# Performance work log

Measured on AMD Instinct MI355X. Metric: run time of the kernel, lower is better.

The kernel has to match this reference:

```python
import jax, jax.numpy as jnp
import numpy as np

N = 64
K_CHEB = 5
EPS = 1e-5

# db4 decomposition filters (scaling_filter.mat Lo_D / Hi_D, length 8)
_LO = np.array([-0.010597401784997278, 0.032883011666982945, 0.030841381835986965,
                -0.18703481171888114, -0.02798376941698385, 0.6308807679295904,
                0.7148465705525415, 0.23037781330885523], dtype=np.float32)
_HI = np.array([-0.23037781330885523, 0.7148465705525415, -0.6308807679295904,
                -0.02798376941698385, 0.18703481171888114, 0.030841381835986965,
                0.032883011666982945, -0.010597401784997278], dtype=np.float32)
# torch stores np.flip(filters) and Conv2d does cross-correlation -> use flipped taps here too
_KERN = np.stack([_LO[::-1], _HI[::-1]])[:, None, None, :].copy()  # [2,1,1,8]


def _wavelet_step(x):
    # x: [B, C, 1, W]; circular pad 3 each side, depthwise len-8 conv, stride 2
    p = 3  # filter_length // 2 - 1
    xp = jnp.concatenate([x[..., -p:], x, x[..., :p]], axis=-1)
    b, c, h, wp = xp.shape
    out = jax.lax.conv_general_dilated(
        xp.reshape(b * c, 1, h, wp), jnp.asarray(_KERN), (1, 2), 'VALID',
        dimension_numbers=('NCHW', 'OIHW', 'NCHW'))
    out = out.reshape(b, c, 2, h, -1)
    return out[:, :, 0], out[:, :, 1]  # (approx, detail)


def _cbam(x, fc1, fc2, sa_w):
    # x: [B, 657, 1, 64]; channel attention then spatial attention
    def mlp(v):  # v: [B, C, 1, 1]
        h = jax.nn.relu(jnp.einsum('oc,bchw->bohw', fc1, v))
        return jnp.einsum('oc,bchw->bohw', fc2, h)
    avg = x.mean(axis=(2, 3), keepdims=True)
    mx = x.max(axis=(2, 3), keepdims=True)
    x = x * jax.nn.sigmoid(mlp(avg) + mlp(mx))
    s = jnp.concatenate([x.mean(axis=1, keepdims=True), x.max(axis=1, keepdims=True)], axis=1)
    sa = jax.nn.sigmoid(jax.lax.conv_general_dilated(
        s, sa_w, (1, 1), ((3, 3), (3, 3)), dimension_numbers=('NCHW', 'OIHW', 'NCHW')))
    return x * sa


def _global_edge_weight(w_tril, mask):
    xs, ys = np.tril_indices(N)
    E = jnp.zeros((N, N), w_tril.dtype).at[xs, ys].set(w_tril)
    E = E + E.T - jnp.diag(jnp.diag(E))
    return (E * mask).reshape(-1)


def _norm_adj(edges, w):
    # PyG NewSGConv.norm: add remaining self-loops (fill=1), deg from |w|, sym normalize
    row, col = edges[0], edges[1]
    has_self = jnp.zeros((N,), w.dtype).at[row].add(jnp.where(row == col, 1.0, 0.0)) > 0
    w_self = jnp.where(has_self, 0.0, 1.0).astype(w.dtype)
    deg = jnp.zeros((N,), w.dtype).at[row].add(jnp.abs(w)) + w_self
    dsafe = jnp.where(deg > 0, deg, 1.0)
    dinv = jnp.where(deg > 0, jax.lax.rsqrt(dsafe), 0.0)
    norm = dinv[row] * w * dinv[col]
    A = jnp.zeros((N, N), w.dtype).at[col, row].add(norm)  # out[i] = sum_j A[i,j] x[j]
    return A + jnp.diag(dinv * w_self * dinv)


def _gcn_block(x, A, W, b, g, be):
    # x: [B, N, C_in]; K-hop SGConv propagation, linear, train-mode batchnorm over (B, N)
    for _ in range(K_CHEB):
        x = jnp.einsum('ij,bjc->bic', A, x)
    x = x @ W.T + b
    mean = x.mean(axis=(0, 1))
    var = x.var(axis=(0, 1))
    return (x - mean) * jax.lax.rsqrt(var + EPS) * g + be


def _classify(x, W1, b1, g, be, W2, b2):
    out = x.reshape(x.shape[0], -1) @ W1.T + b1
    out = (out - out.mean(0)) * jax.lax.rsqrt(out.var(0) + EPS) * g + be
    return jax.nn.log_softmax(out @ W2.T + b2, axis=1)


def _forward(x, local_graph_weight, global_mask, ca_fc1, ca_fc2, sa_conv, edge_weight_tril,
             ld_W, ld_b, ld_g, ld_be, ld1_W, ld1_b, ld1_g, ld1_be,
             d_W, d_b, d_g, d_be, d1_W, d1_b, d1_g, d1_be,
             cls_W1, cls_b1, cls_g, cls_be, cls_W2, cls_b2, edges):
    xc = jnp.transpose(x, (0, 3, 2, 1))        # [B, 657, 1, 64]
    xc = _cbam(xc, ca_fc1, ca_fc2, sa_conv)
    xh = jnp.transpose(xc, (0, 3, 2, 1))       # [B, 64, 1, 657]
    # fi = floor(log2(200)) = 7 -> 4 decomposition levels: 657->328->164->82->41
    out1, _gamma = _wavelet_step(xh)
    out2, _beta = _wavelet_step(out1)
    out3, _alpha = _wavelet_step(out2)
    delta, _theta = _wavelet_step(out3)        # [B, 64, 1, 41]
    delta = delta[:, :, 0, :]                  # squeeze -> [B, 64, 41]
    gw = _global_edge_weight(edge_weight_tril, global_mask)
    A_loc = _norm_adj(edges, local_graph_weight)
    A_glb = _norm_adj(edges, gw)
    lf = _gcn_block(delta, A_loc, ld_W, ld_b, ld_g, ld_be)
    lf = _gcn_block(lf, A_loc, ld1_W, ld1_b, ld1_g, ld1_be)
    gf = _gcn_block(delta, A_glb, d_W, d_b, d_g, d_be)
    gf = _gcn_block(gf, A_glb, d1_W, d1_b, d1_g, d1_be)
    feat = jnp.concatenate([lf.mean(-1, keepdims=True), gf.mean(-1, keepdims=True)], axis=2)  # [B,64,2]
    return _classify(feat, cls_W1, cls_b1, cls_g, cls_be, cls_W2, cls_b2)


def setup_inputs() -> dict:
    key = jax.random.key(0)
    ks = iter(jax.random.split(key, 16))
    B = 512
    f32 = jnp.float32
    def rn(shape, s=0.05):
        return jax.random.normal(next(ks), shape, f32) * s
    ii = jnp.arange(N, dtype=jnp.int32)
    edges = jnp.stack([jnp.repeat(ii, N), jnp.tile(ii, N)])  # full 64x64 mesh (incl. self loops)
    return dict(
        x=jax.random.normal(next(ks), (B, N, 1, 657), f32),
        local_graph_weight=jax.random.uniform(next(ks), (N * N,), f32),
        global_mask=jnp.ones((N, N), f32),
        ca_fc1=rn((82, 657)),
        ca_fc2=rn((657, 82)),
        sa_conv=rn((1, 2, 7, 7), 0.1),
        edge_weight_tril=jax.random.uniform(next(ks), (N * (N + 1) // 2,), f32),
        ld_W=rn((16, 41)), ld_b=jnp.zeros(16, f32), ld_g=jnp.ones(16, f32), ld_be=jnp.zeros(16, f32),
        ld1_W=rn((4, 16)), ld1_b=jnp.zeros(4, f32), ld1_g=jnp.ones(4, f32), ld1_be=jnp.zeros(4, f32),
        d_W=rn((16, 41)), d_b=jnp.zeros(16, f32), d_g=jnp.ones(16, f32), d_be=jnp.zeros(16, f32),
        d1_W=rn((4, 16)), d1_b=jnp.zeros(4, f32), d1_g=jnp.ones(4, f32), d1_be=jnp.zeros(4, f32),
        cls_W1=rn((32, 128)), cls_b1=jnp.zeros(32, f32), cls_g=jnp.ones(32, f32), cls_be=jnp.zeros(32, f32),
        cls_W2=rn((2, 32)), cls_b2=jnp.zeros(2, f32),
        edges=edges,
    )


def reference(x, local_graph_weight, global_mask, ca_fc1, ca_fc2, sa_conv, edge_weight_tril,
              ld_W, ld_b, ld_g, ld_be, ld1_W, ld1_b, ld1_g, ld1_be,
              d_W, d_b, d_g, d_be, d1_W, d1_b, d1_g, d1_be,
              cls_W1, cls_b1, cls_g, cls_be, cls_W2, cls_b2, edges):
    return _forward(x, local_graph_weight, global_mask, ca_fc1, ca_fc2, sa_conv, edge_weight_tril,
                    ld_W, ld_b, ld_g, ld_be, ld1_W, ld1_b, ld1_g, ld1_be,
                    d_W, d_b, d_g, d_be, d1_W, d1_b, d1_g, d1_be,
                    cls_W1, cls_b1, cls_g, cls_be, cls_W2, cls_b2, edges)
```

## Files before the change

### kernel.cpp

```cpp
#include <hip/hip_runtime.h>
#include <math.h>

#define NB 512
#define NN 64
#define TL 657
#define LV1 328
#define LV2 164
#define LV3 82
#define LV4 41
#define HID 82
#define ST 66
#define NGB 32

#define WS_M      0
#define WS_ACC    32768
#define WS_SMEAN  36864
#define WS_SMAX   167936
#define WS_CATT   3373568
#define WS_Y1     682496
#define WS_DELTA  4876800
#define WS_Y2     4876800
#define WS_OUT1   5925376

#define ACC_Y1 0
#define ACC_Y2 64
#define ACC_O1 80

__device__ __forceinline__ float sigmoidf_(float v){ return 1.0f/(1.0f+expf(-v)); }

__device__ __forceinline__ void wav_level(float* __restrict__ dst, const float* __restrict__ src,
                                          int outL, int inL, int lane){
  const float DLO[8] = {0.23037781330885523f, 0.7148465705525415f, 0.6308807679295904f,
                        -0.02798376941698385f, -0.18703481171888114f, 0.030841381835986965f,
                        0.032883011666982945f, -0.010597401784997278f};
  for (int k=lane; k<outL; k+=64){
    int i0 = 2*k - 3;
    float a = 0.f;
    #pragma unroll
    for (int j=0;j<8;j++){
      int idx = i0 + j;
      idx = (idx < 0) ? idx + inL : ((idx >= inL) ? idx - inL : idx);
      a += src[idx]*DLO[j];
    }
    dst[k] = a;
  }
}

__global__ __launch_bounds__(512) void k_front(
    const float* __restrict__ x,
    const float* __restrict__ lgw, const float* __restrict__ gmask,
    const float* __restrict__ tril, const int* __restrict__ edges,
    const float* __restrict__ fc1, const float* __restrict__ fc2,
    float* __restrict__ catt_g,
    float* __restrict__ Mout, double* __restrict__ acc)
{
  __shared__ float smem[3*NN*ST];
  __shared__ float deg[64], hs[64], dinv[64], wself[64];
  int tid = threadIdx.x;
  int bid = blockIdx.x;
  int wv = tid>>6, lane = tid&63;

  if (bid < NGB){
    int g  = bid >> 4;
    int s4 = (bid & 15) * 4;
    float* Wbuf = smem;
    float* Amat = smem + NN*ST;
    float* Rc   = smem + 2*NN*ST;
    float* Rn   = Rc + 4*ST;
    if (bid==0 && tid<512) acc[tid]=0.0;
    for (int e=tid;e<4096;e+=512){
      float w;
      if (g==0) w = lgw[e];
      else {
        int i=e>>6, j=e&63;
        int aa = (i>j)? i:j, bb = (i>j)? j:i;
        w = tril[aa*(aa+1)/2 + bb] * gmask[e];
      }
      Wbuf[e] = w;
    }
    for (int i=tid;i<NN*ST;i+=512) Amat[i] = 0.f;
    if (tid<64){ deg[tid]=0.f; hs[tid]=0.f; }
    __syncthreads();
    {
      int e0 = tid*8;
      int runr = edges[e0];
      float runv = 0.f;
      #pragma unroll
      for (int i=0;i<8;i++){
        int e = e0+i;
        int r = edges[e];
        int c = edges[4096+e];
        float w = Wbuf[e];
        if (r != runr){ atomicAdd(&deg[runr], runv); runr = r; runv = 0.f; }
        runv += fabsf(w);
        if (r == c) hs[r] = 1.f;
      }
      atomicAdd(&deg[runr], runv);
    }
    __syncthreads();
    if (tid<64){
      float w_ = (hs[tid] > 0.f) ? 0.f : 1.f;
      float d = deg[tid] + w_;
      dinv[tid] = (d > 0.f) ? rsqrtf(d) : 0.f;
      wself[tid] = w_;
    }
    __syncthreads();
    for (int e=tid;e<4096;e+=512){
      int r = edges[e], c = edges[4096+e];
      float nm = dinv[r]*Wbuf[e]*dinv[c];
      atomicAdd(&Amat[c*ST+r], nm);
    }
    __syncthreads();
    if (tid<64) Amat[tid*ST+tid] += dinv[tid]*wself[tid]*dinv[tid];
    __syncthreads();
    if (tid < 256){
      int r = tid>>6, c = tid&63;
      Rc[r*ST+c] = Amat[(s4+r)*ST+c];
    }
    __syncthreads();
    #pragma unroll
    for (int it=0; it<4; it++){
      if (tid < 256){
        int r = tid>>6, c = tid&63;
        const float* rr = &Rc[r*ST];
        float a0=0.f, a1=0.f;
        #pragma unroll 8
        for (int k=0;k<64;k+=2){
          a0 += rr[k]  *Amat[k*ST+c];
          a1 += rr[k+1]*Amat[(k+1)*ST+c];
        }
        Rn[r*ST+c] = a0+a1;
      }
      __syncthreads();
      float* t = Rc; Rc = Rn; Rn = t;
    }
    if (tid < 256){
      int r = tid>>6, c = tid&63;
      Mout[g*4096 + (s4+r)*64 + c] = Rc[r*ST+c];
    }
    return;
  }

  int b = bid - NGB;
  {
    float s[11], m[11];
    #pragma unroll
    for (int i=0;i<11;i++){ s[i]=0.f; m[i]=-INFINITY; }
    const float* xb = x + (size_t)b*NN*TL;
    for (int r=0;r<8;r++){
      const float* row = xb + (size_t)(wv*8 + r)*TL;
      #pragma unroll
      for (int i=0;i<11;i++){
        int t = lane + 64*i;
        if (t < TL){
          float v = row[t];
          s[i] += v; m[i] = fmaxf(m[i], v);
        }
      }
    }
    for (int step=4; step>=1; step>>=1){
      if (wv >= step && wv < 2*step){
        float* bs = smem + (wv-step)*1328;
        #pragma unroll
        for (int i=0;i<11;i++){
          int t = lane + 64*i;
          if (t<TL){ bs[t] = s[i]; bs[664+t] = m[i]; }
        }
      }
      __syncthreads();
      if (wv < step){
        float* bs = smem + wv*1328;
        #pragma unroll
        for (int i=0;i<11;i++){
          int t = lane + 64*i;
          if (t<TL){ s[i] += bs[t]; m[i] = fmaxf(m[i], bs[664+t]); }
        }
      }
      __syncthreads();
    }
    float* cs = smem;
    float* cm = smem + 664;
    float* h  = smem + 1400;
    if (wv==0){
      #pragma unroll
      for (int i=0;i<11;i++){
        int t = lane + 64*i;
        if (t<TL){ cs[t] = s[i]; cm[t] = m[i]; }
      }
    }
    __syncthreads();
    for (int o=wv; o<HID; o+=8){
      const float* fr = fc1 + (size_t)o*TL;
      float a = 0.f, bm = 0.f;
      #pragma unroll
      for (int i=0;i<11;i++){
        int c = lane + 64*i;
        if (c < TL){
          float f = fr[c];
          a += f*cs[c]; bm += f*cm[c];
        }
      }
      #pragma unroll
      for (int off=32;off;off>>=1){
        a  += __shfl_xor(a,off);
        bm += __shfl_xor(bm,off);
      }
      if (lane==0)
        h[o] = fmaxf(a*(1.0f/64.0f),0.f) + fmaxf(bm,0.f);
    }
    __syncthreads();
    for (int c=tid; c<TL; c+=512){
      const float2* fr = (const float2*)(fc2 + (size_t)c*HID);
      float a0=0.f, a1=0.f;
      #pragma unroll
      for (int u2=0;u2<41;u2++){
        float2 v = fr[u2];
        a0 += v.x*h[2*u2]; a1 += v.y*h[2*u2+1];
      }
      catt_g[(size_t)b*TL + c] = sigmoidf_(a0+a1);
    }
  }
}

__global__ __launch_bounds__(256) void k_wav(
    const float* __restrict__ x, const float* __restrict__ catt_g,
    float* __restrict__ delta, float* __restrict__ smean, float* __restrict__ smax)
{
  __shared__ float catt[TL];
  __shared__ float yb[4][TL];
  __shared__ float o1b[4][LV1];
  __shared__ float o2b[4][LV2];
  __shared__ float o3b[4][LV3];
  int tid = threadIdx.x, b = blockIdx.x;
  for (int i=tid;i<TL;i+=256) catt[i] = catt_g[(size_t)b*TL + i];
  __syncthreads();
  int wv = tid>>6, lane = tid&63;
  int n = blockIdx.y*4 + wv;
  float* y  = yb[wv];
  float* p1 = o1b[wv];
  float* p2 = o2b[wv];
  float* p3 = o3b[wv];
  const float DLO[8] = {0.23037781330885523f, 0.7148465705525415f, 0.6308807679295904f,
                        -0.02798376941698385f, -0.18703481171888114f, 0.030841381835986965f,
                        0.032883011666982945f, -0.010597401784997278f};
  const float* row = x + ((size_t)b*NN + n)*TL;
  float ls = 0.f, lm = -INFINITY;
  #pragma unroll
  for (int i=0;i<11;i++){
    int t = lane + 64*i;
    if (t < TL){
      float v = row[t]*catt[t];
      y[t] = v; ls += v; lm = fmaxf(lm,v);
    }
  }
  #pragma unroll
  for (int off=32;off;off>>=1){
    ls += __shfl_xor(ls,off);
    lm = fmaxf(lm, __shfl_xor(lm,off));
  }
  if (lane==0){ smean[b*NN+n] = ls*(1.0f/657.0f); smax[b*NN+n] = lm; }
  wav_level(p1, y,  LV1, TL,  lane);
  wav_level(p2, p1, LV2, LV1, lane);
  wav_level(p3, p2, LV3, LV2, lane);
  if (lane < LV4){
    int i0 = 2*lane - 3;
    float a = 0.f;
    #pragma unroll
    for (int j=0;j<8;j++){
      int idx = i0 + j;
      idx = (idx < 0) ? idx + LV3 : ((idx >= LV3) ? idx - LV3 : idx);
      a += p3[idx]*DLO[j];
    }
    delta[((size_t)b*NN + n)*LV4 + lane] = a;
  }
}

__global__ __launch_bounds__(256) void k_gcn1(
  const float* __restrict__ delta, const float* __restrict__ Mmat,
  const float* __restrict__ smean, const float* __restrict__ smax,
  const float* __restrict__ saw,
  const float* __restrict__ ldW, const float* __restrict__ ldb,
  const float* __restrict__ dW, const float* __restrict__ db2,
  float* __restrict__ Y1, double* __restrict__ acc)
{
  __shared__ float Dl[NN*LV4];
  __shared__ float Tt[NN*16];
  __shared__ float Mm[4096];
  __shared__ float Wl[16*LV4];
  __shared__ float satt[NN];
  __shared__ double red[256];
  int tid=threadIdx.x, b=blockIdx.x;
  if (tid < NN){
    float a = 0.f;
    #pragma unroll
    for (int kw=0;kw<7;kw++){
      int w = tid + kw - 3;
      if (0<=w && w<NN) a += smean[b*NN+w]*saw[21+kw] + smax[b*NN+w]*saw[70+kw];
    }
    satt[tid] = sigmoidf_(a);
  }
  __syncthreads();
  const float* ds = delta + (size_t)b*NN*LV4;
  for (int i=tid;i<NN*LV4;i+=256) Dl[i] = ds[i]*satt[i/LV4];
  for (int g=0; g<2; g++){
    const float* Ws = g ? dW : ldW;
    const float* bs = g ? db2 : ldb;
    for (int i=tid;i<16*LV4;i+=256) Wl[i]=Ws[i];
    for (int i=tid;i<4096;i+=256) Mm[i]=Mmat[g*4096+i];
    __syncthreads();
    for (int e=tid;e<NN*16;e+=256){
      int n=e>>4, o=e&15;
      const float* dr=&Dl[n*LV4];
      const float* wr=&Wl[o*LV4];
      float a=0.f;
      #pragma unroll 8
      for (int c=0;c<LV4;c++) a += dr[c]*wr[c];
      Tt[e]=a;
    }
    __syncthreads();
    float bias = bs[tid&15];
    float ps=0.f, pq=0.f;
    for (int m=0;m<4;m++){
      int e=tid+256*m;
      int n=e>>4, o=e&15;
      float a=bias;
      #pragma unroll 8
      for (int k=0;k<64;k++) a += Mm[n*64+k]*Tt[k*16+o];
      Y1[((size_t)b*NN+n)*32 + g*16 + o] = a;
      ps += a; pq += a*a;
    }
    red[tid]=(double)ps;
    __syncthreads();
    if (tid<16){ double t=0; for (int r=tid;r<256;r+=16) t+=red[r]; atomicAdd(&acc[ACC_Y1+g*32+tid], t); }
    __syncthreads();
    red[tid]=(double)pq;
    __syncthreads();
    if (tid<16){ double t=0; for (int r=tid;r<256;r+=16) t+=red[r]; atomicAdd(&acc[ACC_Y1+g*32+16+tid], t); }
    __syncthreads();
  }
}

__global__ __launch_bounds__(256) void k_gcn2(
  const float* __restrict__ Y1, const float* __restrict__ Mmat,
  const float* __restrict__ ldg, const float* __restrict__ ldbe,
  const float* __restrict__ dg, const float* __restrict__ dbe,
  const float* __restrict__ ld1W, const float* __restrict__ ld1b,
  const float* __restrict__ d1W, const float* __restrict__ d1b,
  float* __restrict__ Y2, double* __restrict__ acc)
{
  __shared__ float Yl[NN*32];
  __shared__ float T2[NN*8];
  __shared__ float Mm[2*4096];
  __shared__ float scl[32], sht[32];
  __shared__ double red[256];
  int tid=threadIdx.x, b=blockIdx.x;
  const float* ys = Y1 + (size_t)b*NN*32;
  for (int i=tid;i<NN*32;i+=256) Yl[i]=ys[i];
  for (int i=tid;i<8192;i+=256) Mm[i]=Mmat[i];
  if (tid<32){
    int g=tid>>4, o=tid&15;
    double s=acc[ACC_Y1+g*32+o], q=acc[ACC_Y1+g*32+16+o];
    double mean=s/32768.0;
    double var=q/32768.0 - mean*mean;
    float gam = g? dg[o] : ldg[o];
    float bet = g? dbe[o] : ldbe[o];
    float sc = gam * rsqrtf((float)var + 1e-5f);
    scl[tid]=sc; sht[tid]=bet - (float)mean*sc;
  }
  __syncthreads();
  for (int i=tid;i<NN*32;i+=256){ int c=i&31; Yl[i]=Yl[i]*scl[c]+sht[c]; }
  __syncthreads();
  for (int e=tid;e<NN*8;e+=256){
    int n=e>>3, c=e&7, g=c>>2, p=c&3;
    const float* w = (g? d1W : ld1W) + p*16;
    const float* yr = &Yl[n*32 + g*16];
    float a=0.f;
    #pragma unroll
    for (int o=0;o<16;o++) a += yr[o]*w[o];
    T2[e]=a;
  }
  __syncthreads();
  float ps=0.f,pq=0.f;
  for (int m=0;m<2;m++){
    int e=tid+256*m;
    int n=e>>3, c=e&7, g=c>>2;
    float a = g? d1b[c&3] : ld1b[c&3];
    const float* mr=&Mm[g*4096+n*64];
    #pragma unroll 8
    for (int k=0;k<64;k++) a += mr[k]*T2[k*8+c];
    Y2[((size_t)b*NN+n)*8 + c] = a;
    ps+=a; pq+=a*a;
  }
  red[tid]=(double)ps; __syncthreads();
  if (tid<8){ double t=0; for (int r=tid;r<256;r+=8) t+=red[r]; atomicAdd(&acc[ACC_Y2 + (tid>>2)*8 + (tid&3)], t); }
  __syncthreads();
  red[tid]=(double)pq; __syncthreads();
  if (tid<8){ double t=0; for (int r=tid;r<256;r+=8) t+=red[r]; atomicAdd(&acc[ACC_Y2 + (tid>>2)*8 + 4 + (tid&3)], t); }
}

__global__ __launch_bounds__(64) void k_featcls(
  const float* __restrict__ Y2,
  const float* __restrict__ ld1g, const float* __restrict__ ld1be,
  const float* __restrict__ d1g, const float* __restrict__ d1be,
  const float* __restrict__ W1, const float* __restrict__ b1,
  float* __restrict__ out1, double* __restrict__ acc)
{
  __shared__ float f[128];
  __shared__ float scl[8], sht[8];
  int tid=threadIdx.x, b=blockIdx.x;
  if (tid<8){
    int g=tid>>2, p=tid&3;
    double s=acc[ACC_Y2+g*8+p], q=acc[ACC_Y2+g*8+4+p];
    double mean=s/32768.0;
    double var=q/32768.0-mean*mean;
    float gam = g? d1g[p]:ld1g[p];
    float bet = g? d1be[p]:ld1be[p];
    float sc = gam*rsqrtf((float)var+1e-5f);
    scl[tid]=sc; sht[tid]=bet-(float)mean*sc;
  }
  __syncthreads();
  {
    const float* yr = Y2 + ((size_t)b*NN+tid)*8;
    float lf=0.f, gf=0.f;
    #pragma unroll
    for (int p=0;p<4;p++){
      lf += yr[p]*scl[p]+sht[p];
      gf += yr[4+p]*scl[4+p]+sht[4+p];
    }
    f[2*tid]   = lf*0.25f;
    f[2*tid+1] = gf*0.25f;
  }
  __syncthreads();
  if (tid<32){
    const float* w = W1 + tid*128;
    float a = b1[tid];
    #pragma unroll 4
    for (int m=0;m<128;m++) a += w[m]*f[m];
    out1[b*32+tid]=a;
    atomicAdd(&acc[ACC_O1+tid], (double)a);
    atomicAdd(&acc[ACC_O1+32+tid], (double)(a*a));
  }
}

__global__ __launch_bounds__(64) void k_cls2(
  const float* __restrict__ out1,
  const float* __restrict__ cg, const float* __restrict__ cbe,
  const float* __restrict__ W2, const float* __restrict__ b2,
  const double* __restrict__ acc, float* __restrict__ out)
{
  __shared__ float v[32];
  __shared__ float z[2];
  int tid=threadIdx.x, b=blockIdx.x;
  if (tid<32){
    double s=acc[ACC_O1+tid], q=acc[ACC_O1+32+tid];
    double mean=s/512.0;
    double var=q/512.0-mean*mean;
    float sc=cg[tid]*rsqrtf((float)var+1e-5f);
    float sh=cbe[tid]-(float)mean*sc;
    v[tid]=out1[b*32+tid]*sc+sh;
  }
  __syncthreads();
  if (tid<2){
    const float* w=W2+tid*32;
    float a=b2[tid];
    #pragma unroll
    for (int j=0;j<32;j++) a += w[j]*v[j];
    z[tid]=a;
  }
  __syncthreads();
  if (tid<2){
    float m=fmaxf(z[0],z[1]);
    float l=m+logf(expf(z[0]-m)+expf(z[1]-m));
    out[b*2+tid]=z[tid]-l;
  }
}

extern "C" void kernel_launch(void* const* d_in, const int* in_sizes, int n_in,
                              void* d_out, int out_size, void* d_ws, size_t ws_size,
                              hipStream_t stream) {
  (void)in_sizes; (void)n_in; (void)out_size; (void)ws_size;
  const float* x     = (const float*)d_in[0];
  const float* lgw   = (const float*)d_in[1];
  const float* gmask = (const float*)d_in[2];
  const float* fc1   = (const float*)d_in[3];
  const float* fc2   = (const float*)d_in[4];
  const float* saw   = (const float*)d_in[5];
  const float* tril  = (const float*)d_in[6];
  const float* ldW   = (const float*)d_in[7];
  const float* ldb   = (const float*)d_in[8];
  const float* ldg   = (const float*)d_in[9];
  const float* ldbe  = (const float*)d_in[10];
  const float* ld1W  = (const float*)d_in[11];
  const float* ld1b  = (const float*)d_in[12];
  const float* ld1g  = (const float*)d_in[13];
  const float* ld1be = (const float*)d_in[14];
  const float* dW    = (const float*)d_in[15];
  const float* db2   = (const float*)d_in[16];
  const float* dg    = (const float*)d_in[17];
  const float* dbe   = (const float*)d_in[18];
  const float* d1W   = (const float*)d_in[19];
  const float* d1b   = (const float*)d_in[20];
  const float* d1g   = (const float*)d_in[21];
  const float* d1be  = (const float*)d_in[22];
  const float* cW1   = (const float*)d_in[23];
  const float* cb1   = (const float*)d_in[24];
  const float* cgam  = (const float*)d_in[25];
  const float* cbet  = (const float*)d_in[26];
  const float* cW2   = (const float*)d_in[27];
  const float* cb2   = (const float*)d_in[28];
  const int*   edges = (const int*)d_in[29];

  char* ws = (char*)d_ws;
  float*  M     = (float*)(ws + WS_M);
  double* acc   = (double*)(ws + WS_ACC);
  float*  smean = (float*)(ws + WS_SMEAN);
  float*  smax  = (float*)(ws + WS_SMAX);
  float*  catt  = (float*)(ws + WS_CATT);
  float*  Y1    = (float*)(ws + WS_Y1);
  float*  delta = (float*)(ws + WS_DELTA);
  float*  Y2    = (float*)(ws + WS_Y2);
  float*  out1  = (float*)(ws + WS_OUT1);
  float*  out   = (float*)d_out;

  k_front<<<NB + NGB, 512, 0, stream>>>(x, lgw, gmask, tril, edges, fc1, fc2,
                                        catt, M, acc);
  k_wav<<<dim3(NB, 16), 256, 0, stream>>>(x, catt, delta, smean, smax);
  k_gcn1<<<NB, 256, 0, stream>>>(delta, M, smean, smax, saw, ldW, ldb, dW, db2, Y1, acc);
  k_gcn2<<<NB, 256, 0, stream>>>(Y1, M, ldg, ldbe, dg, dbe, ld1W, ld1b, d1W, d1b, Y2, acc);
  k_featcls<<<NB, 64, 0, stream>>>(Y2, ld1g, ld1be, d1g, d1be, cW1, cb1, out1, acc);
  k_cls2<<<NB, 64, 0, stream>>>(out1, cgam, cbet, cW2, cb2, acc, out);
}
```

Baseline: 168.4 us.

## Fuse wavelet kernel into front kernel with fp16 shared-memory copy of x

Merges the channel-attention front kernel and the wavelet decomposition kernel into one block per batch item. The block loads each batch's x once into shared memory as fp16, then reuses it for the reductions and the wavelet stage, so x is no longer read twice from global memory and the catt round-trip through global memory goes away. The costs are large LDS use (about 84KB fp16 plus buffers), which limits occupancy, 8 rows handled serially per wave instead of spread over 16x grid blocks, and reduced precision of x.

```diff
diff --git a/kernel.cpp b/kernel.cpp
--- a/kernel.cpp
+++ b/kernel.cpp
@@ -1,4 +1,5 @@
 #include <hip/hip_runtime.h>
+#include <hip/hip_fp16.h>
 #include <math.h>
 
 #define NB 512
@@ -16,7 +17,6 @@
 #define WS_ACC    32768
 #define WS_SMEAN  36864
 #define WS_SMAX   167936
-#define WS_CATT   3373568
 #define WS_Y1     682496
 #define WS_DELTA  4876800
 #define WS_Y2     4876800
@@ -51,11 +51,13 @@
     const float* __restrict__ lgw, const float* __restrict__ gmask,
     const float* __restrict__ tril, const int* __restrict__ edges,
     const float* __restrict__ fc1, const float* __restrict__ fc2,
-    float* __restrict__ catt_g,
-    float* __restrict__ Mout, double* __restrict__ acc)
+    float* __restrict__ Mout, double* __restrict__ acc,
+    float* __restrict__ delta, float* __restrict__ smean, float* __restrict__ smax)
 {
-  __shared__ float smem[3*NN*ST];
-  __shared__ float deg[64], hs[64], dinv[64], wself[64];
+  __shared__ __half xs[NN*TL];
+  __shared__ float wbuf[8][1240];
+  __shared__ float cs[TL], cm[TL], catt[TL], h[HID];
+  __shared__ float deg[64], hsv[64], dinv[64], wself[64];
   int tid = threadIdx.x;
   int bid = blockIdx.x;
   int wv = tid>>6, lane = tid&63;
@@ -63,9 +65,9 @@
   if (bid < NGB){
     int g  = bid >> 4;
     int s4 = (bid & 15) * 4;
-    float* Wbuf = smem;
-    float* Amat = smem + NN*ST;
-    float* Rc   = smem + 2*NN*ST;
+    float* Wbuf = (float*)xs;
+    float* Amat = Wbuf + 4096;
+    float* Rc   = Amat + NN*ST;
     float* Rn   = Rc + 4*ST;
     if (bid==0 && tid<512) acc[tid]=0.0;
     for (int e=tid;e<4096;e+=512){
@@ -79,7 +81,7 @@
       Wbuf[e] = w;
     }
     for (int i=tid;i<NN*ST;i+=512) Amat[i] = 0.f;
-    if (tid<64){ deg[tid]=0.f; hs[tid]=0.f; }
+    if (tid<64){ deg[tid]=0.f; hsv[tid]=0.f; }
     __syncthreads();
     {
       int e0 = tid*8;
@@ -93,13 +95,13 @@
         float w = Wbuf[e];
         if (r != runr){ atomicAdd(&deg[runr], runv); runr = r; runv = 0.f; }
         runv += fabsf(w);
-        if (r == c) hs[r] = 1.f;
+        if (r == c) hsv[r] = 1.f;
       }
       atomicAdd(&deg[runr], runv);
     }
     __syncthreads();
     if (tid<64){
-      float w_ = (hs[tid] > 0.f) ? 0.f : 1.f;
+      float w_ = (hsv[tid] > 0.f) ? 0.f : 1.f;
       float d = deg[tid] + w_;
       dinv[tid] = (d > 0.f) ? rsqrtf(d) : 0.f;
       wself[tid] = w_;
@@ -142,25 +144,44 @@
   }
 
   int b = bid - NGB;
+  const float* xb = x + (size_t)b*NN*TL;
+
+  #pragma unroll
+  for (int g2=0; g2<2; ++g2){
+    int grp = wv*2 + g2;
+    const float4* src = (const float4*)(xb + grp*2628);
+    #pragma unroll
+    for (int it=0; it<11; ++it){
+      int f = lane + 64*it;
+      if (f < 657){
+        float4 v = src[f];
+        __half2 p0; p0.x = __float2half(v.x); p0.y = __float2half(v.y);
+        __half2 p1; p1.x = __float2half(v.z); p1.y = __float2half(v.w);
+        __half2* dst = (__half2*)&xs[grp*2628 + 4*f];
+        dst[0] = p0; dst[1] = p1;
+      }
+    }
+  }
+
   {
     float s[11], m[11];
     #pragma unroll
     for (int i=0;i<11;i++){ s[i]=0.f; m[i]=-INFINITY; }
-    const float* xb = x + (size_t)b*NN*TL;
-    for (int r=0;r<8;r++){
-      const float* row = xb + (size_t)(wv*8 + r)*TL;
+    for (int rr=0; rr<8; ++rr){
+      const __half* xr = &xs[(wv*8+rr)*TL];
       #pragma unroll
       for (int i=0;i<11;i++){
         int t = lane + 64*i;
         if (t < TL){
-          float v = row[t];
+          float v = __half2float(xr[t]);
           s[i] += v; m[i] = fmaxf(m[i], v);
         }
       }
     }
+    float* mrg = &wbuf[0][0];
     for (int step=4; step>=1; step>>=1){
       if (wv >= step && wv < 2*step){
-        float* bs = smem + (wv-step)*1328;
+        float* bs = mrg + (wv-step)*1328;
         #pragma unroll
         for (int i=0;i<11;i++){
           int t = lane + 64*i;
@@ -169,7 +190,7 @@
       }
       __syncthreads();
       if (wv < step){
-        float* bs = smem + wv*1328;
+        float* bs = mrg + wv*1328;
         #pragma unroll
         for (int i=0;i<11;i++){
           int t = lane + 64*i;
@@ -178,9 +199,6 @@
       }
       __syncthreads();
     }
-    float* cs = smem;
-    float* cm = smem + 664;
-    float* h  = smem + 1400;
     if (wv==0){
       #pragma unroll
       for (int i=0;i<11;i++){
@@ -189,89 +207,81 @@
       }
     }
     __syncthreads();
-    for (int o=wv; o<HID; o+=8){
-      const float* fr = fc1 + (size_t)o*TL;
-      float a = 0.f, bm = 0.f;
+  }
+
+  for (int o=wv; o<HID; o+=8){
+    const float* fr = fc1 + (size_t)o*TL;
+    float a = 0.f, bm = 0.f;
+    #pragma unroll
+    for (int i=0;i<11;i++){
+      int c = lane + 64*i;
+      if (c < TL){
+        float f = fr[c];
+        a += f*cs[c]; bm += f*cm[c];
+      }
+    }
+    #pragma unroll
+    for (int off=32;off;off>>=1){
+      a  += __shfl_xor(a,off);
+      bm += __shfl_xor(bm,off);
+    }
+    if (lane==0)
+      h[o] = fmaxf(a*(1.0f/64.0f),0.f) + fmaxf(bm,0.f);
+  }
+  __syncthreads();
+  for (int c=tid; c<TL; c+=512){
+    const float2* fr = (const float2*)(fc2 + (size_t)c*HID);
+    float a0=0.f, a1=0.f;
+    #pragma unroll
+    for (int u2=0;u2<41;u2++){
+      float2 v = fr[u2];
+      a0 += v.x*h[2*u2]; a1 += v.y*h[2*u2+1];
+    }
+    catt[c] = sigmoidf_(a0+a1);
+  }
+  __syncthreads();
+
+  {
+    float* y  = &wbuf[wv][0];
+    float* o1 = &wbuf[wv][660];
+    float* o2 = &wbuf[wv][988];
+    float* o3 = &wbuf[wv][1152];
+    const float DLO[8] = {0.23037781330885523f, 0.7148465705525415f, 0.6308807679295904f,
+                          -0.02798376941698385f, -0.18703481171888114f, 0.030841381835986965f,
+                          0.032883011666982945f, -0.010597401784997278f};
+    for (int rr=0; rr<8; ++rr){
+      int n = wv*8 + rr;
+      const __half* xr = &xs[n*TL];
+      float ls = 0.f, lm = -INFINITY;
       #pragma unroll
       for (int i=0;i<11;i++){
-        int c = lane + 64*i;
-        if (c < TL){
-          float f = fr[c];
-          a += f*cs[c]; bm += f*cm[c];
+        int t = lane + 64*i;
+        if (t < TL){
+          float v = __half2float(xr[t])*catt[t];
+          y[t] = v; ls += v; lm = fmaxf(lm,v);
         }
       }
       #pragma unroll
       for (int off=32;off;off>>=1){
-        a  += __shfl_xor(a,off);
-        bm += __shfl_xor(bm,off);
-      }
-      if (lane==0)
-        h[o] = fmaxf(a*(1.0f/64.0f),0.f) + fmaxf(bm,0.f);
-    }
-    __syncthreads();
-    for (int c=tid; c<TL; c+=512){
-      const float2* fr = (const float2*)(fc2 + (size_t)c*HID);
-      float a0=0.f, a1=0.f;
-      #pragma unroll
-      for (int u2=0;u2<41;u2++){
-        float2 v = fr[u2];
-        a0 += v.x*h[2*u2]; a1 += v.y*h[2*u2+1];
-      }
-      catt_g[(size_t)b*TL + c] = sigmoidf_(a0+a1);
-    }
-  }
-}
-
-__global__ __launch_bounds__(256) void k_wav(
-    const float* __restrict__ x, const float* __restrict__ catt_g,
-    float* __restrict__ delta, float* __restrict__ smean, float* __restrict__ smax)
-{
-  __shared__ float catt[TL];
-  __shared__ float yb[4][TL];
-  __shared__ float o1b[4][LV1];
-  __shared__ float o2b[4][LV2];
-  __shared__ float o3b[4][LV3];
-  int tid = threadIdx.x, b = blockIdx.x;
-  for (int i=tid;i<TL;i+=256) catt[i] = catt_g[(size_t)b*TL + i];
-  __syncthreads();
-  int wv = tid>>6, lane = tid&63;
-  int n = blockIdx.y*4 + wv;
-  float* y  = yb[wv];
-  float* p1 = o1b[wv];
-  float* p2 = o2b[wv];
-  float* p3 = o3b[wv];
-  const float DLO[8] = {0.23037781330885523f, 0.7148465705525415f, 0.6308807679295904f,
-                        -0.02798376941698385f, -0.18703481171888114f, 0.030841381835986965f,
-                        0.032883011666982945f, -0.010597401784997278f};
-  const float* row = x + ((size_t)b*NN + n)*TL;
-  float ls = 0.f, lm = -INFINITY;
-  #pragma unroll
-  for (int i=0;i<11;i++){
-    int t = lane + 64*i;
-    if (t < TL){
-      float v = row[t]*catt[t];
-      y[t] = v; ls += v; lm = fmaxf(lm,v);
-    }
-  }
-  #pragma unroll
-  for (int off=32;off;off>>=1){
-    ls += __shfl_xor(ls,off);
-    lm = fmaxf(lm, __shfl_xor(lm,off));
-  }
-  if (lane==0){ smean[b*NN+n] = ls*(1.0f/657.0f); smax[b*NN+n] = lm; }
-  wav_level(p1, y,  LV1, TL,  lane);
-  wav_level(p2, p1, LV2, LV1, lane);
-  wav_level(p3, p2, LV3, LV2, lane);
-  if (lane < LV4){
-    int i0 = 2*lane - 3;
-    float a = 0.f;
-    #pragma unroll
-    for (int j=0;j<8;j++){
-      int idx = i0 + j;
-      idx = (idx < 0) ? idx + LV3 : ((idx >= LV3) ? idx - LV3 : idx);
-      a += p3[idx]*DLO[j];
-    }
-    delta[((size_t)b*NN + n)*LV4 + lane] = a;
+        ls += __shfl_xor(ls,off);
+        lm = fmaxf(lm, __shfl_xor(lm,off));
+      }
+      if (lane==0){ smean[b*NN+n] = ls*(1.0f/657.0f); smax[b*NN+n] = lm; }
+      wav_level(o1, y,  LV1, TL,  lane);
+      wav_level(o2, o1, LV2, LV1, lane);
+      wav_level(o3, o2, LV3, LV2, lane);
+      if (lane < LV4){
+        int i0 = 2*lane - 3;
+        float a = 0.f;
+        #pragma unroll
+        for (int j=0;j<8;j++){
+          int idx = i0 + j;
+          idx = (idx < 0) ? idx + LV3 : ((idx >= LV3) ? idx - LV3 : idx);
+          a += o3[idx]*DLO[j];
+        }
+        delta[((size_t)b*NN + n)*LV4 + lane] = a;
+      }
+    }
   }
 }
 
@@ -515,7 +525,6 @@
   double* acc   = (double*)(ws + WS_ACC);
   float*  smean = (float*)(ws + WS_SMEAN);
   float*  smax  = (float*)(ws + WS_SMAX);
-  float*  catt  = (float*)(ws + WS_CATT);
   float*  Y1    = (float*)(ws + WS_Y1);
   float*  delta = (float*)(ws + WS_DELTA);
   float*  Y2    = (float*)(ws + WS_Y2);
@@ -523,8 +532,7 @@
   float*  out   = (float*)d_out;
 
   k_front<<<NB + NGB, 512, 0, stream>>>(x, lgw, gmask, tril, edges, fc1, fc2,
-                                        catt, M, acc);
-  k_wav<<<dim3(NB, 16), 256, 0, stream>>>(x, catt, delta, smean, smax);
+                                        M, acc, delta, smean, smax);
   k_gcn1<<<NB, 256, 0, stream>>>(delta, M, smean, smax, saw, ldW, ldb, dW, db2, Y1, acc);
   k_gcn2<<<NB, 256, 0, stream>>>(Y1, M, ldg, ldbe, dg, dbe, ld1W, ld1b, d1W, d1b, Y2, acc);
   k_featcls<<<NB, 64, 0, stream>>>(Y2, ld1g, ld1be, d1g, d1be, cW1, cb1, out1, acc);
```

Result: slower. 174.6 us (+3.7%).

## Vectorize x reads with float4 and stage rows through padded shared buffers

Applied to the files above, without the earlier changes.

The front kernel's per-batch channel reduction now reads x as float4, treating the batch's 64 rows as a flat array. Each thread accumulates sum and max over 16 strided groups, then 4 partial rows are combined in shared memory, replacing the 8-wave tree reduction. The wavelet kernel loads its 4 rows at once as float4 into a padded shared buffer, splitting the elements that cross row boundaries, and the GCN kernels copy M and Y with float4. The aim is fewer, wider global loads and fewer barriers, at the cost of more complex indexing and a larger shared footprint.

```diff
diff --git a/kernel.cpp b/kernel.cpp
--- a/kernel.cpp
+++ b/kernel.cpp
@@ -54,8 +54,8 @@
     float* __restrict__ catt_g,
     float* __restrict__ Mout, double* __restrict__ acc)
 {
-  __shared__ float smem[3*NN*ST];
-  __shared__ float deg[64], hs[64], dinv[64], wself[64];
+  __shared__ float smem[8848];
+  __shared__ float deg[64], hsv[64], dinv[64], wself[64];
   int tid = threadIdx.x;
   int bid = blockIdx.x;
   int wv = tid>>6, lane = tid&63;
@@ -64,9 +64,9 @@
     int g  = bid >> 4;
     int s4 = (bid & 15) * 4;
     float* Wbuf = smem;
-    float* Amat = smem + NN*ST;
-    float* Rc   = smem + 2*NN*ST;
-    float* Rn   = Rc + 4*ST;
+    float* Amat = smem + 4096;
+    float* Rc   = smem + 8320;
+    float* Rn   = smem + 8584;
     if (bid==0 && tid<512) acc[tid]=0.0;
     for (int e=tid;e<4096;e+=512){
       float w;
@@ -79,7 +79,7 @@
       Wbuf[e] = w;
     }
     for (int i=tid;i<NN*ST;i+=512) Amat[i] = 0.f;
-    if (tid<64){ deg[tid]=0.f; hs[tid]=0.f; }
+    if (tid<64){ deg[tid]=0.f; hsv[tid]=0.f; }
     __syncthreads();
     {
       int e0 = tid*8;
@@ -93,13 +93,13 @@
         float w = Wbuf[e];
         if (r != runr){ atomicAdd(&deg[runr], runv); runr = r; runv = 0.f; }
         runv += fabsf(w);
-        if (r == c) hs[r] = 1.f;
+        if (r == c) hsv[r] = 1.f;
       }
       atomicAdd(&deg[runr], runv);
     }
     __syncthreads();
     if (tid<64){
-      float w_ = (hs[tid] > 0.f) ? 0.f : 1.f;
+      float w_ = (hsv[tid] > 0.f) ? 0.f : 1.f;
       float d = deg[tid] + w_;
       dinv[tid] = (d > 0.f) ? rsqrtf(d) : 0.f;
       wself[tid] = w_;
@@ -142,83 +142,72 @@
   }
 
   int b = bid - NGB;
-  {
-    float s[11], m[11];
-    #pragma unroll
-    for (int i=0;i<11;i++){ s[i]=0.f; m[i]=-INFINITY; }
-    const float* xb = x + (size_t)b*NN*TL;
-    for (int r=0;r<8;r++){
-      const float* row = xb + (size_t)(wv*8 + r)*TL;
-      #pragma unroll
-      for (int i=0;i<11;i++){
-        int t = lane + 64*i;
-        if (t < TL){
-          float v = row[t];
-          s[i] += v; m[i] = fmaxf(m[i], v);
-        }
+  const float4* xb4 = (const float4*)(x + (size_t)b*NN*TL);
+  int f0 = tid;
+  int f1 = 512 + tid;
+  bool has1 = (f1 < 657);
+  float4 S0 = make_float4(0.f,0.f,0.f,0.f);
+  float4 M0 = make_float4(-INFINITY,-INFINITY,-INFINITY,-INFINITY);
+  float4 S1 = S0, M1 = M0;
+  #pragma unroll 4
+  for (int g=0; g<16; ++g){
+    float4 v = xb4[g*657 + f0];
+    S0.x += v.x; S0.y += v.y; S0.z += v.z; S0.w += v.w;
+    M0.x = fmaxf(M0.x, v.x); M0.y = fmaxf(M0.y, v.y);
+    M0.z = fmaxf(M0.z, v.z); M0.w = fmaxf(M0.w, v.w);
+    if (has1){
+      float4 w = xb4[g*657 + f1];
+      S1.x += w.x; S1.y += w.y; S1.z += w.z; S1.w += w.w;
+      M1.x = fmaxf(M1.x, w.x); M1.y = fmaxf(M1.y, w.y);
+      M1.z = fmaxf(M1.z, w.z); M1.w = fmaxf(M1.w, w.w);
+    }
+  }
+  float* Sf = smem;
+  float* Mf = smem + 2628;
+  float* cs = smem + 5256;
+  float* cm = smem + 5916;
+  float* h  = smem + 6576;
+  *(float4*)&Sf[4*f0] = S0;
+  *(float4*)&Mf[4*f0] = M0;
+  if (has1){
+    *(float4*)&Sf[4*f1] = S1;
+    *(float4*)&Mf[4*f1] = M1;
+  }
+  __syncthreads();
+  for (int c=tid; c<TL; c+=512){
+    cs[c] = (Sf[c] + Sf[c+657]) + (Sf[c+1314] + Sf[c+1971]);
+    cm[c] = fmaxf(fmaxf(Mf[c], Mf[c+657]), fmaxf(Mf[c+1314], Mf[c+1971]));
+  }
+  __syncthreads();
+  for (int o=wv; o<HID; o+=8){
+    const float* fr = fc1 + (size_t)o*TL;
+    float a = 0.f, bm = 0.f;
+    #pragma unroll
+    for (int i=0;i<11;i++){
+      int c = lane + 64*i;
+      if (c < TL){
+        float f = fr[c];
+        a += f*cs[c]; bm += f*cm[c];
       }
     }
-    for (int step=4; step>=1; step>>=1){
-      if (wv >= step && wv < 2*step){
-        float* bs = smem + (wv-step)*1328;
-        #pragma unroll
-        for (int i=0;i<11;i++){
-          int t = lane + 64*i;
-          if (t<TL){ bs[t] = s[i]; bs[664+t] = m[i]; }
-        }
-      }
-      __syncthreads();
-      if (wv < step){
-        float* bs = smem + wv*1328;
-        #pragma unroll
-        for (int i=0;i<11;i++){
-          int t = lane + 64*i;
-          if (t<TL){ s[i] += bs[t]; m[i] = fmaxf(m[i], bs[664+t]); }
-        }
-      }
-      __syncthreads();
-    }
-    float* cs = smem;
-    float* cm = smem + 664;
-    float* h  = smem + 1400;
-    if (wv==0){
-      #pragma unroll
-      for (int i=0;i<11;i++){
-        int t = lane + 64*i;
-        if (t<TL){ cs[t] = s[i]; cm[t] = m[i]; }
-      }
-    }
-    __syncthreads();
-    for (int o=wv; o<HID; o+=8){
-      const float* fr = fc1 + (size_t)o*TL;
-      float a = 0.f, bm = 0.f;
-      #pragma unroll
-      for (int i=0;i<11;i++){
-        int c = lane + 64*i;
-        if (c < TL){
-          float f = fr[c];
-          a += f*cs[c]; bm += f*cm[c];
-        }
-      }
-      #pragma unroll
-      for (int off=32;off;off>>=1){
-        a  += __shfl_xor(a,off);
-        bm += __shfl_xor(bm,off);
-      }
-      if (lane==0)
-        h[o] = fmaxf(a*(1.0f/64.0f),0.f) + fmaxf(bm,0.f);
-    }
-    __syncthreads();
-    for (int c=tid; c<TL; c+=512){
-      const float2* fr = (const float2*)(fc2 + (size_t)c*HID);
-      float a0=0.f, a1=0.f;
-      #pragma unroll
-      for (int u2=0;u2<41;u2++){
-        float2 v = fr[u2];
-        a0 += v.x*h[2*u2]; a1 += v.y*h[2*u2+1];
-      }
-      catt_g[(size_t)b*TL + c] = sigmoidf_(a0+a1);
-    }
+    #pragma unroll
+    for (int off=32;off;off>>=1){
+      a  += __shfl_xor(a,off);
+      bm += __shfl_xor(bm,off);
+    }
+    if (lane==0)
+      h[o] = fmaxf(a*(1.0f/64.0f),0.f) + fmaxf(bm,0.f);
+  }
+  __syncthreads();
+  for (int c=tid; c<TL; c+=512){
+    const float2* fr = (const float2*)(fc2 + (size_t)c*HID);
+    float a0=0.f, a1=0.f;
+    #pragma unroll
+    for (int u2=0;u2<41;u2++){
+      float2 v = fr[u2];
+      a0 += v.x*h[2*u2]; a1 += v.y*h[2*u2+1];
+    }
+    catt_g[(size_t)b*TL + c] = sigmoidf_(a0+a1);
   }
 }
 
@@ -226,31 +215,42 @@
     const float* __restrict__ x, const float* __restrict__ catt_g,
     float* __restrict__ delta, float* __restrict__ smean, float* __restrict__ smax)
 {
-  __shared__ float catt[TL];
-  __shared__ float yb[4][TL];
-  __shared__ float o1b[4][LV1];
-  __shared__ float o2b[4][LV2];
-  __shared__ float o3b[4][LV3];
-  int tid = threadIdx.x, b = blockIdx.x;
+  __shared__ float catt[660];
+  __shared__ float buf[2664];
+  __shared__ float o1b[4][332];
+  __shared__ float o2b[4][166];
+  __shared__ float o3b[4][84];
+  int tid = threadIdx.x, b = blockIdx.x, q = blockIdx.y;
   for (int i=tid;i<TL;i+=256) catt[i] = catt_g[(size_t)b*TL + i];
   __syncthreads();
+  const float4* g4 = (const float4*)(x + ((size_t)b*NN + q*4)*TL);
+  for (int f=tid; f<657; f+=256){
+    float4 v = g4[f];
+    int e = 4*f;
+    if (f==164 || f==328 || f==492){
+      float ev[4] = {v.x, v.y, v.z, v.w};
+      #pragma unroll
+      for (int j=0;j<4;j++){
+        int ee = e+j;
+        int r = (ee>=657) + (ee>=1314) + (ee>=1971);
+        buf[ee + 12*r] = ev[j];
+      }
+    } else {
+      int r = (e>=657) + (e>=1314) + (e>=1971);
+      *(float4*)&buf[e + 12*r] = v;
+    }
+  }
+  __syncthreads();
   int wv = tid>>6, lane = tid&63;
-  int n = blockIdx.y*4 + wv;
-  float* y  = yb[wv];
-  float* p1 = o1b[wv];
-  float* p2 = o2b[wv];
-  float* p3 = o3b[wv];
-  const float DLO[8] = {0.23037781330885523f, 0.7148465705525415f, 0.6308807679295904f,
-                        -0.02798376941698385f, -0.18703481171888114f, 0.030841381835986965f,
-                        0.032883011666982945f, -0.010597401784997278f};
-  const float* row = x + ((size_t)b*NN + n)*TL;
+  int n = q*4 + wv;
+  float* y = &buf[669*wv];
   float ls = 0.f, lm = -INFINITY;
   #pragma unroll
   for (int i=0;i<11;i++){
     int t = lane + 64*i;
     if (t < TL){
-      float v = row[t]*catt[t];
-      y[t] = v; ls += v; lm = fmaxf(lm,v);
+      float vv = y[t]*catt[t];
+      y[t] = vv; ls += vv; lm = fmaxf(lm,vv);
     }
   }
   #pragma unroll
@@ -259,17 +259,20 @@
     lm = fmaxf(lm, __shfl_xor(lm,off));
   }
   if (lane==0){ smean[b*NN+n] = ls*(1.0f/657.0f); smax[b*NN+n] = lm; }
-  wav_level(p1, y,  LV1, TL,  lane);
-  wav_level(p2, p1, LV2, LV1, lane);
-  wav_level(p3, p2, LV3, LV2, lane);
+  wav_level(o1b[wv], y,       LV1, TL,  lane);
+  wav_level(o2b[wv], o1b[wv], LV2, LV1, lane);
+  wav_level(o3b[wv], o2b[wv], LV3, LV2, lane);
   if (lane < LV4){
+    const float DLO[8] = {0.23037781330885523f, 0.7148465705525415f, 0.6308807679295904f,
+                          -0.02798376941698385f, -0.18703481171888114f, 0.030841381835986965f,
+                          0.032883011666982945f, -0.010597401784997278f};
     int i0 = 2*lane - 3;
     float a = 0.f;
     #pragma unroll
     for (int j=0;j<8;j++){
       int idx = i0 + j;
       idx = (idx < 0) ? idx + LV3 : ((idx >= LV3) ? idx - LV3 : idx);
-      a += p3[idx]*DLO[j];
+      a += o3b[wv][idx]*DLO[j];
     }
     delta[((size_t)b*NN + n)*LV4 + lane] = a;
   }
@@ -306,7 +309,8 @@
     const float* Ws = g ? dW : ldW;
     const float* bs = g ? db2 : ldb;
     for (int i=tid;i<16*LV4;i+=256) Wl[i]=Ws[i];
-    for (int i=tid;i<4096;i+=256) Mm[i]=Mmat[g*4096+i];
+    const float4* Mm4 = (const float4*)(Mmat + g*4096);
+    for (int i=tid;i<1024;i+=256) *(float4*)&Mm[4*i] = Mm4[i];
     __syncthreads();
     for (int e=tid;e<NN*16;e+=256){
       int n=e>>4, o=e&15;
@@ -354,9 +358,10 @@
   __shared__ float scl[32], sht[32];
   __shared__ double red[256];
   int tid=threadIdx.x, b=blockIdx.x;
-  const float* ys = Y1 + (size_t)b*NN*32;
-  for (int i=tid;i<NN*32;i+=256) Yl[i]=ys[i];
-  for (int i=tid;i<8192;i+=256) Mm[i]=Mmat[i];
+  const float4* ys4 = (const float4*)(Y1 + (size_t)b*NN*32);
+  for (int i=tid;i<512;i+=256) *(float4*)&Yl[4*i] = ys4[i];
+  const float4* Mm4 = (const float4*)Mmat;
+  for (int i=tid;i<2048;i+=256) *(float4*)&Mm[4*i] = Mm4[i];
   if (tid<32){
     int g=tid>>4, o=tid&15;
     double s=acc[ACC_Y1+g*32+o], q=acc[ACC_Y1+g*32+16+o];
```

After: 168.2 us. No clear change (-0.2%).
